# Performance work log

Measured on AMD Instinct MI355X. Metric: run time of the kernel, lower is better.

The kernel has to match this reference:

```python
import jax, jax.numpy as jnp
import numpy as np


def setup_inputs() -> dict:
    key = jax.random.key(0)
    k1, k2, k3, k4, k5 = jax.random.split(key, 5)
    B, S, H, NL = 256, 128, 768, 2
    return {
        "t_logits": jax.random.normal(k1, (B, NL), dtype=jnp.float32),
        "s_logits": jax.random.normal(k2, (B, NL), dtype=jnp.float32),
        "t_features": jax.random.normal(k3, (B, S, H), dtype=jnp.float32),
        "s_features": jax.random.normal(k4, (B, S, H), dtype=jnp.float32),
        "labels": jax.random.randint(k5, (B,), 0, NL, dtype=jnp.int64),
        "k": 5,
        "temperature": 4,
    }


def reference(t_logits, s_logits, t_features, s_features, labels, k, temperature):
    B = s_features.shape[0]
    D = s_features.shape[1] * s_features.shape[2]  # flattened feature dim S*H
    T = jnp.asarray(temperature, dtype=s_logits.dtype)

    # train_loss: standard cross-entropy computed inside the student model
    logp = jax.nn.log_softmax(s_logits, axis=-1)
    train_loss = -jnp.mean(jnp.take_along_axis(logp, labels[:, None].astype(jnp.int32), axis=1))

    # soft_loss: KL(batchmean) between temperature-softened teacher/student
    soft_targets = jax.nn.softmax(t_logits / T, axis=-1)
    log_probs = jax.nn.log_softmax(s_logits / T, axis=-1)
    soft_loss = jnp.sum(soft_targets * (jnp.log(soft_targets) - log_probs)) / B * T * T

    # distill_loss: per-sample squared distances to label-matched teacher
    # features, take k nearest (self included, dist 0), sum of per-neighbor
    # MSE = sqdist / D.
    tf = t_features.reshape(B, -1)
    sf = s_features.reshape(B, -1)
    # ||s_i - t_j||^2 via GEMM: [B, B]
    sq = (jnp.sum(sf * sf, axis=1)[:, None]
          + jnp.sum(tf * tf, axis=1)[None, :]
          - 2.0 * sf @ tf.T)
    sq = jnp.maximum(sq, 0.0)
    same = labels[:, None] == labels[None, :]
    masked = jnp.where(same, sq, jnp.inf)
    neg_top, _ = jax.lax.top_k(-masked, k)  # k smallest distances per row
    vals = -neg_top
    valid = jnp.isfinite(vals)  # handles groups smaller than k
    distill_loss = jnp.sum(jnp.where(valid, vals, 0.0)) / D

    return train_loss, soft_loss, distill_loss
```

## Files before the change

### kernel.cpp

```cpp
#include <hip/hip_runtime.h>
#include <math.h>


#define BM 128
#define BN 128
#define BKF 32
#define STAGE (BM * BKF)

typedef __attribute__((ext_vector_type(8))) short short8;
typedef __attribute__((ext_vector_type(4))) float f32x4;

__device__ inline void async16(const float* g, float* l) {
    __builtin_amdgcn_global_load_lds(
        (const __attribute__((address_space(1))) void*)g,
        (__attribute__((address_space(3))) void*)l,
        16, 0, 0);
}

__device__ inline unsigned pack_trunc(float a, float b) {
    return (__float_as_uint(a) >> 16) | (__float_as_uint(b) & 0xffff0000u);
}

union U8 { short8 v; unsigned u[4]; };

__global__ __launch_bounds__(256) void gemm_dot_kernel(const float* __restrict__ S,
                                                       const float* __restrict__ T,
                                                       float* __restrict__ part,
                                                       float* __restrict__ spart,
                                                       float* __restrict__ tpart,
                                                       int* __restrict__ counter,
                                                       int B, int K, int KC) {
    extern __shared__ __align__(16) float smem[];

    const int tid  = threadIdx.x;
    const int i0   = blockIdx.x * BM;
    const int j0   = blockIdx.y * BN;
    const int bz   = blockIdx.z;
    const int kbeg = bz * KC;
    const int kend = kbeg + KC;

    if (blockIdx.x == 0 && blockIdx.y == 0 && bz == 0 && tid == 0)
        *counter = 0;

    const int lane = tid & 63;
    const int wid  = tid >> 6;
    const int wm   = wid >> 1;
    const int wn   = wid & 1;
    const int l15  = lane & 15;
    const int quad = lane >> 4;

    const int rl = lane >> 3;
    const int p  = lane & 7;
    const float* srcA[4];
    const float* srcB[4];
    int dstOff[4];
    #pragma unroll
    for (int j = 0; j < 4; ++j) {
        const int c   = wid * 4 + j;
        const int row = c * 8 + rl;
        const int g   = p ^ (row & 7);
        int gi = i0 + row; if (gi >= B) gi = B - 1;
        int gj = j0 + row; if (gj >= B) gj = B - 1;
        srcA[j] = S + (size_t)gi * K + kbeg + g * 4;
        srcB[j] = T + (size_t)gj * K + kbeg + g * 4;
        dstOff[j] = c * 256;
    }

    int aoff[4], boff[4];
    #pragma unroll
    for (int t = 0; t < 4; ++t) {
        const int ra = wm * 64 + t * 16 + l15;
        aoff[t] = ra * BKF + (((2 * quad) ^ (ra & 7)) * 4);
        const int rb = wn * 64 + t * 16 + l15;
        boff[t] = rb * BKF + (((2 * quad) ^ (rb & 7)) * 4);
    }

    const bool doS = (blockIdx.y == 0);
    const bool doT = (blockIdx.x == 0);
    const int  rn  = tid >> 1;
    const int  hn  = tid & 1;

    f32x4 acc[4][4] = {};
    float pns = 0.f, pnt = 0.f;

    {
        float* As0 = smem;
        float* Bs0 = smem + STAGE;
        #pragma unroll
        for (int j = 0; j < 4; ++j) {
            async16(srcA[j], &As0[dstOff[j]]);
            async16(srcB[j], &Bs0[dstOff[j]]);
            srcA[j] += BKF;
            srcB[j] += BKF;
        }
    }

    int par = 0;
    for (int kb = kbeg; kb < kend; kb += BKF) {
        __syncthreads();

        if (kb + BKF < kend) {
            float* Asn = smem + (par ^ 1) * 2 * STAGE;
            float* Bsn = Asn + STAGE;
            #pragma unroll
            for (int j = 0; j < 4; ++j) {
                async16(srcA[j], &Asn[dstOff[j]]);
                async16(srcB[j], &Bsn[dstOff[j]]);
                srcA[j] += BKF;
                srcB[j] += BKF;
            }
        }

        const float* As = smem + par * 2 * STAGE;
        const float* Bs = As + STAGE;

        if (doS) {
            #pragma unroll
            for (int j = 0; j < 4; ++j) {
                const int pos = hn * 4 + ((j + rn) & 3);
                f32x4 v = *(const f32x4*)&As[rn * BKF + pos * 4];
                pns += v.x * v.x + v.y * v.y + v.z * v.z + v.w * v.w;
            }
        }
        if (doT) {
            #pragma unroll
            for (int j = 0; j < 4; ++j) {
                const int pos = hn * 4 + ((j + rn) & 3);
                f32x4 v = *(const f32x4*)&Bs[rn * BKF + pos * 4];
                pnt += v.x * v.x + v.y * v.y + v.z * v.z + v.w * v.w;
            }
        }

        short8 af[4], bf[4];
        #pragma unroll
        for (int t = 0; t < 4; ++t) {
            f32x4 va = *(const f32x4*)&As[aoff[t]];
            f32x4 vb = *(const f32x4*)&As[aoff[t] ^ 4];
            U8 u;
            u.u[0] = pack_trunc(va.x, va.y);
            u.u[1] = pack_trunc(va.z, va.w);
            u.u[2] = pack_trunc(vb.x, vb.y);
            u.u[3] = pack_trunc(vb.z, vb.w);
            af[t] = u.v;
        }
        #pragma unroll
        for (int t = 0; t < 4; ++t) {
            f32x4 va = *(const f32x4*)&Bs[boff[t]];
            f32x4 vb = *(const f32x4*)&Bs[boff[t] ^ 4];
            U8 u;
            u.u[0] = pack_trunc(va.x, va.y);
            u.u[1] = pack_trunc(va.z, va.w);
            u.u[2] = pack_trunc(vb.x, vb.y);
            u.u[3] = pack_trunc(vb.z, vb.w);
            bf[t] = u.v;
        }
        #pragma unroll
        for (int mi = 0; mi < 4; ++mi)
            #pragma unroll
            for (int ni = 0; ni < 4; ++ni)
                acc[mi][ni] = __builtin_amdgcn_mfma_f32_16x16x32_bf16(
                    af[mi], bf[ni], acc[mi][ni], 0, 0, 0);

        par ^= 1;
    }

    float* outp = part + (size_t)bz * B * B;
    #pragma unroll
    for (int mi = 0; mi < 4; ++mi) {
        #pragma unroll
        for (int ni = 0; ni < 4; ++ni) {
            #pragma unroll
            for (int r = 0; r < 4; ++r) {
                const int ig = i0 + wm * 64 + mi * 16 + quad * 4 + r;
                const int jg = j0 + wn * 64 + ni * 16 + l15;
                if (ig < B && jg < B)
                    outp[(size_t)ig * B + jg] = acc[mi][ni][r];
            }
        }
    }

    if (doS) {
        float v = pns + __shfl_xor(pns, 1, 64);
        if (hn == 0 && i0 + rn < B) spart[(size_t)bz * B + i0 + rn] = v;
    }
    if (doT) {
        float v = pnt + __shfl_xor(pnt, 1, 64);
        if (hn == 0 && j0 + rn < B) tpart[(size_t)bz * B + j0 + rn] = v;
    }
}

__global__ __launch_bounds__(256) void tail_kernel(const float* __restrict__ part,
                                                   const float* __restrict__ spart,
                                                   const float* __restrict__ tpart,
                                                   const float* __restrict__ t_logits,
                                                   const float* __restrict__ s_logits,
                                                   const int* __restrict__ labels,
                                                   const int* __restrict__ kp,
                                                   const int* __restrict__ tp,
                                                   float* __restrict__ rowsum,
                                                   int* __restrict__ counter,
                                                   float* __restrict__ out,
                                                   int B, int K, int NL, int gz) {
    const int i   = blockIdx.x;
    const int tid = threadIdx.x;
    const size_t BB = (size_t)B * B;

    __shared__ float svals[256];
    __shared__ float rv[256];
    __shared__ int   ri[256];
    __shared__ float red[4];
    __shared__ float snv;
    __shared__ int   lastf;

    float sp = 0.f;
    for (int z = tid; z < gz; z += 256) sp += spart[(size_t)z * B + i];
    #pragma unroll
    for (int off = 32; off > 0; off >>= 1) sp += __shfl_down(sp, off, 64);
    if ((tid & 63) == 0) red[tid >> 6] = sp;
    __syncthreads();
    if (tid == 0) snv = red[0] + red[1] + red[2] + red[3];
    __syncthreads();
    const float sn = snv;

    float v = INFINITY;
    if (tid < B) {
        const float* pp = part + (size_t)i * B + tid;
        const float* tq = tpart + tid;
        float d0=0.f,d1=0.f,d2=0.f,d3=0.f,d4=0.f,d5=0.f,d6=0.f,d7=0.f;
        float tn = 0.f;
        int z = 0;
        for (; z + 8 <= gz; z += 8) {
            d0 += pp[(size_t)(z+0) * BB];
            d1 += pp[(size_t)(z+1) * BB];
            d2 += pp[(size_t)(z+2) * BB];
            d3 += pp[(size_t)(z+3) * BB];
            d4 += pp[(size_t)(z+4) * BB];
            d5 += pp[(size_t)(z+5) * BB];
            d6 += pp[(size_t)(z+6) * BB];
            d7 += pp[(size_t)(z+7) * BB];
            tn += tq[(size_t)(z+0) * B] + tq[(size_t)(z+1) * B]
                + tq[(size_t)(z+2) * B] + tq[(size_t)(z+3) * B]
                + tq[(size_t)(z+4) * B] + tq[(size_t)(z+5) * B]
                + tq[(size_t)(z+6) * B] + tq[(size_t)(z+7) * B];
        }
        float dt = ((d0+d1)+(d2+d3)) + ((d4+d5)+(d6+d7));
        for (; z < gz; ++z) {
            dt += pp[(size_t)z * BB];
            tn += tq[(size_t)z * B];
        }
        if (labels[i] == labels[tid])
            v = fmaxf(sn + tn - 2.0f * dt, 0.0f);
    }
    svals[tid] = v;
    __syncthreads();

    const int k = kp[0];
    float sum = 0.0f;
    for (int it = 0; it < k; ++it) {
        rv[tid] = svals[tid];
        ri[tid] = tid;
        __syncthreads();
        #pragma unroll
        for (int s = 128; s > 0; s >>= 1) {
            if (tid < s) {
                if (rv[tid + s] < rv[tid]) { rv[tid] = rv[tid + s]; ri[tid] = ri[tid + s]; }
            }
            __syncthreads();
        }
        if (tid == 0) {
            if (rv[0] < 3.0e38f) sum += rv[0];
            svals[ri[0]] = INFINITY;
        }
        __syncthreads();
    }

    if (tid == 0) {
        rowsum[i] = sum;
        __threadfence();
        lastf = (atomicAdd(counter, 1) == B - 1) ? 1 : 0;
    }
    __syncthreads();
    if (!lastf) return;

    __threadfence();
    const float Tv = (float)tp[0];
    float rs = (tid < B) ? rowsum[tid] : 0.f;
    float ce = 0.0f, kl = 0.0f;
    for (int s = tid; s < B; s += 256) {
        const float* sl = s_logits + (size_t)s * NL;
        const float* tl = t_logits + (size_t)s * NL;
        float mx = -INFINITY;
        for (int c = 0; c < NL; ++c) mx = fmaxf(mx, sl[c]);
        float se = 0.0f;
        for (int c = 0; c < NL; ++c) se += expf(sl[c] - mx);
        ce += logf(se) + mx - sl[labels[s]];

        float mxs = -INFINITY, mxt = -INFINITY;
        for (int c = 0; c < NL; ++c) {
            mxs = fmaxf(mxs, sl[c] / Tv);
            mxt = fmaxf(mxt, tl[c] / Tv);
        }
        float ses = 0.0f, set = 0.0f;
        for (int c = 0; c < NL; ++c) {
            ses += expf(sl[c] / Tv - mxs);
            set += expf(tl[c] / Tv - mxt);
        }
        float lses = logf(ses) + mxs;
        float lset = logf(set) + mxt;
        for (int c = 0; c < NL; ++c) {
            float lst = tl[c] / Tv - lset;
            float ls  = sl[c] / Tv - lses;
            kl += expf(lst) * (lst - ls);
        }
    }
    #pragma unroll
    for (int off = 32; off > 0; off >>= 1) {
        ce += __shfl_down(ce, off, 64);
        kl += __shfl_down(kl, off, 64);
        rs += __shfl_down(rs, off, 64);
    }
    __shared__ float wce[4], wkl[4], wrs[4];
    if ((tid & 63) == 0) { wce[tid >> 6] = ce; wkl[tid >> 6] = kl; wrs[tid >> 6] = rs; }
    __syncthreads();
    if (tid == 0) {
        out[0] = (wce[0] + wce[1] + wce[2] + wce[3]) / (float)B;
        out[1] = (wkl[0] + wkl[1] + wkl[2] + wkl[3]) / (float)B * Tv * Tv;
        out[2] = (wrs[0] + wrs[1] + wrs[2] + wrs[3]) / (float)K;
    }
}

extern "C" void kernel_launch(void* const* d_in, const int* in_sizes, int n_in,
                              void* d_out, int out_size, void* d_ws, size_t ws_size,
                              hipStream_t stream) {
    const float* t_logits = (const float*)d_in[0];
    const float* s_logits = (const float*)d_in[1];
    const float* t_feat   = (const float*)d_in[2];
    const float* s_feat   = (const float*)d_in[3];
    const int*   labels   = (const int*)d_in[4];
    const int*   kp       = (const int*)d_in[5];
    const int*   tp       = (const int*)d_in[6];
    float* out = (float*)d_out;

    const int B  = in_sizes[4];
    const int NL = in_sizes[0] / B;
    const int K  = in_sizes[2] / B;
    const size_t BB = (size_t)B * B;

    const size_t avail = ws_size / 4;
    const int cands[] = {192, 256, 128, 96, 64, 48, 32, 24, 16, 12, 8, 6, 4, 3, 2, 1};
    int gz = 1;
    for (int ci = 0; ci < 16; ++ci) {
        const int g = cands[ci];
        if (K % (g * BKF) != 0) continue;
        const size_t need = (size_t)g * BB + 2 * (size_t)g * B + B + 1;
        if (need <= avail) { gz = g; break; }
    }
    const int KC = K / gz;

    float* ws      = (float*)d_ws;
    float* part    = ws;
    float* spart   = part + (size_t)gz * BB;
    float* tpart   = spart + (size_t)gz * B;
    float* rowsum  = tpart + (size_t)gz * B;
    int*   counter = (int*)(rowsum + B);

    dim3 grid((B + BM - 1) / BM, (B + BN - 1) / BN, gz);
    const size_t lds_bytes = 4 * STAGE * sizeof(float);
    gemm_dot_kernel<<<grid, 256, lds_bytes, stream>>>(s_feat, t_feat, part,
                                                      spart, tpart, counter,
                                                      B, K, KC);

    tail_kernel<<<B, 256, 0, stream>>>(part, spart, tpart, t_logits, s_logits,
                                       labels, kp, tp, rowsum, counter, out,
                                       B, K, NL, gz);
}
```

Before: 272.3 us.

## Use one 1024-thread block per K-split covering the full 256x256 tile with bf16 LDS staging

Replaces the 2x2 grid of 128x128 tiles per K-split with a single 1024-thread block that computes the whole 256x256 product per split. Each S/T row is now read from global memory once per split instead of twice. Features are loaded into registers, converted to bf16 with round-to-nearest, and written to a double-buffered LDS, which halves LDS footprint and removes the repeated fp32-to-bf16 packing per wave. Squared norms are computed in registers for every block. The trade-offs are that async global-to-LDS loads become synchronous register loads with software prefetch, the tile now hard-codes B<=256, and the largest K-split count changes.

```diff
diff --git a/kernel.cpp b/kernel.cpp
--- a/kernel.cpp
+++ b/kernel.cpp
@@ -2,166 +2,104 @@
 #include <math.h>
 
 
-#define BM 128
-#define BN 128
-#define BKF 32
-#define STAGE (BM * BKF)
+#define BMAC 256
+#define BKF  32
+#define LP   32
+#define ST   (BMAC * LP)
 
 typedef __attribute__((ext_vector_type(8))) short short8;
 typedef __attribute__((ext_vector_type(4))) float f32x4;
 
-__device__ inline void async16(const float* g, float* l) {
-    __builtin_amdgcn_global_load_lds(
-        (const __attribute__((address_space(1))) void*)g,
-        (__attribute__((address_space(3))) void*)l,
-        16, 0, 0);
+__device__ inline unsigned pack_bf16(float a, float b) {
+    unsigned ua = __float_as_uint(a), ub = __float_as_uint(b);
+    ua = (ua + 0x7fffu + ((ua >> 16) & 1u)) >> 16;
+    ub = (ub + 0x7fffu + ((ub >> 16) & 1u)) >> 16;
+    return (ua & 0xffffu) | (ub << 16);
 }
 
-__device__ inline unsigned pack_trunc(float a, float b) {
-    return (__float_as_uint(a) >> 16) | (__float_as_uint(b) & 0xffff0000u);
-}
-
-union U8 { short8 v; unsigned u[4]; };
-
-__global__ __launch_bounds__(256) void gemm_dot_kernel(const float* __restrict__ S,
-                                                       const float* __restrict__ T,
-                                                       float* __restrict__ part,
-                                                       float* __restrict__ spart,
-                                                       float* __restrict__ tpart,
-                                                       int* __restrict__ counter,
-                                                       int B, int K, int KC) {
-    extern __shared__ __align__(16) float smem[];
+__global__ __launch_bounds__(1024) void gemm_dot_kernel(const float* __restrict__ S,
+                                                        const float* __restrict__ T,
+                                                        float* __restrict__ part,
+                                                        float* __restrict__ spart,
+                                                        float* __restrict__ tpart,
+                                                        int* __restrict__ counter,
+                                                        int B, int K, int KC) {
+    extern __shared__ __align__(16) unsigned short smem[];
 
     const int tid  = threadIdx.x;
-    const int i0   = blockIdx.x * BM;
-    const int j0   = blockIdx.y * BN;
-    const int bz   = blockIdx.z;
+    const int bz   = blockIdx.x;
     const int kbeg = bz * KC;
-    const int kend = kbeg + KC;
-
-    if (blockIdx.x == 0 && blockIdx.y == 0 && bz == 0 && tid == 0)
-        *counter = 0;
+    const int iters = KC / BKF;
+
+    if (bz == 0 && tid == 0) *counter = 0;
+
+    const int r = tid >> 2;
+    const int g = tid & 3;
+    int gi = r < B ? r : B - 1;
+    const float* srcS = S + (size_t)gi * K + kbeg + g * 8;
+    const float* srcT = T + (size_t)gi * K + kbeg + g * 8;
+    const int woff = r * LP + ((g ^ (r & 3)) * 8);
 
     const int lane = tid & 63;
     const int wid  = tid >> 6;
-    const int wm   = wid >> 1;
-    const int wn   = wid & 1;
+    const int wm   = wid >> 2;
+    const int wn   = wid & 3;
     const int l15  = lane & 15;
     const int quad = lane >> 4;
-
-    const int rl = lane >> 3;
-    const int p  = lane & 7;
-    const float* srcA[4];
-    const float* srcB[4];
-    int dstOff[4];
-    #pragma unroll
-    for (int j = 0; j < 4; ++j) {
-        const int c   = wid * 4 + j;
-        const int row = c * 8 + rl;
-        const int g   = p ^ (row & 7);
-        int gi = i0 + row; if (gi >= B) gi = B - 1;
-        int gj = j0 + row; if (gj >= B) gj = B - 1;
-        srcA[j] = S + (size_t)gi * K + kbeg + g * 4;
-        srcB[j] = T + (size_t)gj * K + kbeg + g * 4;
-        dstOff[j] = c * 256;
-    }
-
+    const int xq   = (quad ^ (l15 & 3)) * 8;
     int aoff[4], boff[4];
     #pragma unroll
     for (int t = 0; t < 4; ++t) {
-        const int ra = wm * 64 + t * 16 + l15;
-        aoff[t] = ra * BKF + (((2 * quad) ^ (ra & 7)) * 4);
-        const int rb = wn * 64 + t * 16 + l15;
-        boff[t] = rb * BKF + (((2 * quad) ^ (rb & 7)) * 4);
-    }
-
-    const bool doS = (blockIdx.y == 0);
-    const bool doT = (blockIdx.x == 0);
-    const int  rn  = tid >> 1;
-    const int  hn  = tid & 1;
+        aoff[t] = (wm * 64 + t * 16 + l15) * LP + xq;
+        boff[t] = (wn * 64 + t * 16 + l15) * LP + xq;
+    }
 
     f32x4 acc[4][4] = {};
     float pns = 0.f, pnt = 0.f;
 
-    {
-        float* As0 = smem;
-        float* Bs0 = smem + STAGE;
+    f32x4 s0 = *(const f32x4*)srcS;
+    f32x4 s1 = *(const f32x4*)(srcS + 4);
+    f32x4 t0 = *(const f32x4*)srcT;
+    f32x4 t1 = *(const f32x4*)(srcT + 4);
+
+    for (int it = 0; it < iters; ++it) {
+        unsigned short* As = smem + (it & 1) * 2 * ST;
+        unsigned short* Bs = As + ST;
+
+        pns += s0.x*s0.x + s0.y*s0.y + s0.z*s0.z + s0.w*s0.w
+             + s1.x*s1.x + s1.y*s1.y + s1.z*s1.z + s1.w*s1.w;
+        pnt += t0.x*t0.x + t0.y*t0.y + t0.z*t0.z + t0.w*t0.w
+             + t1.x*t1.x + t1.y*t1.y + t1.z*t1.z + t1.w*t1.w;
+        uint4 pa = make_uint4(pack_bf16(s0.x, s0.y), pack_bf16(s0.z, s0.w),
+                              pack_bf16(s1.x, s1.y), pack_bf16(s1.z, s1.w));
+        uint4 pb = make_uint4(pack_bf16(t0.x, t0.y), pack_bf16(t0.z, t0.w),
+                              pack_bf16(t1.x, t1.y), pack_bf16(t1.z, t1.w));
+        *(uint4*)&As[woff] = pa;
+        *(uint4*)&Bs[woff] = pb;
+
+        if (it + 1 < iters) {
+            const float* nS = srcS + (it + 1) * BKF;
+            const float* nT = srcT + (it + 1) * BKF;
+            s0 = *(const f32x4*)nS;
+            s1 = *(const f32x4*)(nS + 4);
+            t0 = *(const f32x4*)nT;
+            t1 = *(const f32x4*)(nT + 4);
+        }
+
+        __syncthreads();
+
+        short8 bfr[4];
         #pragma unroll
-        for (int j = 0; j < 4; ++j) {
-            async16(srcA[j], &As0[dstOff[j]]);
-            async16(srcB[j], &Bs0[dstOff[j]]);
-            srcA[j] += BKF;
-            srcB[j] += BKF;
-        }
-    }
-
-    int par = 0;
-    for (int kb = kbeg; kb < kend; kb += BKF) {
-        __syncthreads();
-
-        if (kb + BKF < kend) {
-            float* Asn = smem + (par ^ 1) * 2 * STAGE;
-            float* Bsn = Asn + STAGE;
-            #pragma unroll
-            for (int j = 0; j < 4; ++j) {
-                async16(srcA[j], &Asn[dstOff[j]]);
-                async16(srcB[j], &Bsn[dstOff[j]]);
-                srcA[j] += BKF;
-                srcB[j] += BKF;
-            }
-        }
-
-        const float* As = smem + par * 2 * STAGE;
-        const float* Bs = As + STAGE;
-
-        if (doS) {
-            #pragma unroll
-            for (int j = 0; j < 4; ++j) {
-                const int pos = hn * 4 + ((j + rn) & 3);
-                f32x4 v = *(const f32x4*)&As[rn * BKF + pos * 4];
-                pns += v.x * v.x + v.y * v.y + v.z * v.z + v.w * v.w;
-            }
-        }
-        if (doT) {
-            #pragma unroll
-            for (int j = 0; j < 4; ++j) {
-                const int pos = hn * 4 + ((j + rn) & 3);
-                f32x4 v = *(const f32x4*)&Bs[rn * BKF + pos * 4];
-                pnt += v.x * v.x + v.y * v.y + v.z * v.z + v.w * v.w;
-            }
-        }
-
-        short8 af[4], bf[4];
+        for (int ni = 0; ni < 4; ++ni)
+            bfr[ni] = *(const short8*)&Bs[boff[ni]];
         #pragma unroll
-        for (int t = 0; t < 4; ++t) {
-            f32x4 va = *(const f32x4*)&As[aoff[t]];
-            f32x4 vb = *(const f32x4*)&As[aoff[t] ^ 4];
-            U8 u;
-            u.u[0] = pack_trunc(va.x, va.y);
-            u.u[1] = pack_trunc(va.z, va.w);
-            u.u[2] = pack_trunc(vb.x, vb.y);
-            u.u[3] = pack_trunc(vb.z, vb.w);
-            af[t] = u.v;
-        }
-        #pragma unroll
-        for (int t = 0; t < 4; ++t) {
-            f32x4 va = *(const f32x4*)&Bs[boff[t]];
-            f32x4 vb = *(const f32x4*)&Bs[boff[t] ^ 4];
-            U8 u;
-            u.u[0] = pack_trunc(va.x, va.y);
-            u.u[1] = pack_trunc(va.z, va.w);
-            u.u[2] = pack_trunc(vb.x, vb.y);
-            u.u[3] = pack_trunc(vb.z, vb.w);
-            bf[t] = u.v;
-        }
-        #pragma unroll
-        for (int mi = 0; mi < 4; ++mi)
+        for (int mi = 0; mi < 4; ++mi) {
+            short8 afr = *(const short8*)&As[aoff[mi]];
             #pragma unroll
             for (int ni = 0; ni < 4; ++ni)
                 acc[mi][ni] = __builtin_amdgcn_mfma_f32_16x16x32_bf16(
-                    af[mi], bf[ni], acc[mi][ni], 0, 0, 0);
-
-        par ^= 1;
+                    afr, bfr[ni], acc[mi][ni], 0, 0, 0);
+        }
     }
 
     float* outp = part + (size_t)bz * B * B;
@@ -170,22 +108,24 @@
         #pragma unroll
         for (int ni = 0; ni < 4; ++ni) {
             #pragma unroll
-            for (int r = 0; r < 4; ++r) {
-                const int ig = i0 + wm * 64 + mi * 16 + quad * 4 + r;
-                const int jg = j0 + wn * 64 + ni * 16 + l15;
+            for (int rr = 0; rr < 4; ++rr) {
+                const int ig = wm * 64 + mi * 16 + quad * 4 + rr;
+                const int jg = wn * 64 + ni * 16 + l15;
                 if (ig < B && jg < B)
-                    outp[(size_t)ig * B + jg] = acc[mi][ni][r];
+                    outp[(size_t)ig * B + jg] = acc[mi][ni][rr];
             }
         }
     }
 
-    if (doS) {
-        float v = pns + __shfl_xor(pns, 1, 64);
-        if (hn == 0 && i0 + rn < B) spart[(size_t)bz * B + i0 + rn] = v;
-    }
-    if (doT) {
-        float v = pnt + __shfl_xor(pnt, 1, 64);
-        if (hn == 0 && j0 + rn < B) tpart[(size_t)bz * B + j0 + rn] = v;
+    {
+        float v = pns;
+        v += __shfl_xor(v, 1, 64);
+        v += __shfl_xor(v, 2, 64);
+        if ((tid & 3) == 0 && r < B) spart[(size_t)bz * B + r] = v;
+        float w = pnt;
+        w += __shfl_xor(w, 1, 64);
+        w += __shfl_xor(w, 2, 64);
+        if ((tid & 3) == 0 && r < B) tpart[(size_t)bz * B + r] = w;
     }
 }
 
@@ -347,9 +287,9 @@
     const size_t BB = (size_t)B * B;
 
     const size_t avail = ws_size / 4;
-    const int cands[] = {192, 256, 128, 96, 64, 48, 32, 24, 16, 12, 8, 6, 4, 3, 2, 1};
-    int gz = 1;
-    for (int ci = 0; ci < 16; ++ci) {
+    const int cands[] = {256, 192, 128, 96, 64, 48, 32, 24, 16, 12, 8, 6, 4};
+    int gz = 4;
+    for (int ci = 0; ci < 13; ++ci) {
         const int g = cands[ci];
         if (K % (g * BKF) != 0) continue;
         const size_t need = (size_t)g * BB + 2 * (size_t)g * B + B + 1;
@@ -364,11 +304,10 @@
     float* rowsum  = tpart + (size_t)gz * B;
     int*   counter = (int*)(rowsum + B);
 
-    dim3 grid((B + BM - 1) / BM, (B + BN - 1) / BN, gz);
-    const size_t lds_bytes = 4 * STAGE * sizeof(float);
-    gemm_dot_kernel<<<grid, 256, lds_bytes, stream>>>(s_feat, t_feat, part,
-                                                      spart, tpart, counter,
-                                                      B, K, KC);
+    const size_t lds_bytes = 2 * 2 * (size_t)ST * sizeof(unsigned short);
+    gemm_dot_kernel<<<gz, 1024, lds_bytes, stream>>>(s_feat, t_feat, part,
+                                                     spart, tpart, counter,
+                                                     B, K, KC);
 
     tail_kernel<<<B, 256, 0, stream>>>(part, spart, tpart, t_logits, s_logits,
                                        labels, kp, tp, rowsum, counter, out,
```

After: 276.1 us. Within noise of the previous version (+1.4%).
